# Performance work log

Measured on AMD Instinct MI355X. Metric: run time of the kernel, lower is better.

## Reference

```python
import jax, jax.numpy as jnp
import numpy as np

B, N, H, W, D = 4, 8, 32, 32, 64

def setup_inputs() -> dict:
    key = jax.random.key(0)
    k1, k2, k3, k4 = jax.random.split(key, 4)
    scale = D ** (-0.5)
    q = jax.random.normal(k1, (B, N, H, W, D), dtype=jnp.float32)
    k = jax.random.normal(k2, (B, N, H, W, D), dtype=jnp.float32)
    # learned absolute position embeddings, init N(mean=scale, std=1) per nn.init.normal_(t, scale)
    ph = jax.random.normal(k3, (H, D), dtype=jnp.float32) + scale
    pw = jax.random.normal(k4, (W, D), dtype=jnp.float32) + scale
    return {"q": q, "k": k, "ph": ph, "pw": pw}

def reference(q, k, ph, pw):
    # content-content logits: [b,n,H,W,H,W]
    logits = jnp.einsum('bnhwd,bnpqd->bnhwpq', q, k)
    # absolute positional bias: emb[p,q,d] = ph[p,d] + pw[q,d]
    emb = ph[:, None, :] + pw[None, :, :]            # [H, W, D]
    logits = logits + jnp.einsum('bnxyd,pqd->bnxypq', q, emb)
    return logits
```

## Files before the change

### kernel.cpp

```cpp
#include <hip/hip_runtime.h>


typedef __bf16 bf16x8 __attribute__((ext_vector_type(8)));
typedef __bf16 bf16x4 __attribute__((ext_vector_type(4)));
typedef float  f32x16 __attribute__((ext_vector_type(16)));

#define LDSTRIDE 72

__global__ __launch_bounds__(512)
void abs_pos_emb_gemm(const float* __restrict__ q,
                      const float* __restrict__ k,
                      const float* __restrict__ ph,
                      const float* __restrict__ pw,
                      float* __restrict__ out)
{
    extern __shared__ __bf16 lds[];
    __bf16* As  = lds;
    __bf16* Bs0 = lds + 256 * LDSTRIDE;
    __bf16* Bs1 = lds + 320 * LDSTRIDE;

    const int tid = threadIdx.x;
    const int bid = blockIdx.x;
    const int batch = ((bid & 7) << 2) + (bid >> 6);
    const int j     = (bid >> 3) & 7;
    const int trow  = (j >> 1) << 8;
    const int tcol0 = (j & 1) << 9;

    const float* Qb = q + (size_t)batch * (1024 * 64);
    const float* Kb = k + (size_t)batch * (1024 * 64);
    float* Ob = out + (size_t)batch * (1024u * 1024u);

#pragma unroll
    for (int i = 0; i < 8; ++i) {
        int f   = i * 512 + tid;
        int row = f >> 4;
        int col = (f & 15) << 2;
        float4 v = *reinterpret_cast<const float4*>(
            Qb + (size_t)(trow + row) * 64 + col);
        bf16x4 h;
        h[0] = (__bf16)v.x; h[1] = (__bf16)v.y;
        h[2] = (__bf16)v.z; h[3] = (__bf16)v.w;
        *reinterpret_cast<bf16x4*>(&As[row * LDSTRIDE + col]) = h;
    }

#pragma unroll
    for (int i = 0; i < 2; ++i) {
        int f   = i * 512 + tid;
        int row = f >> 4;
        int col = (f & 15) << 2;
        int grow = tcol0 + row;
        int p  = grow >> 5;
        int qq = grow & 31;
        float4 v  = *reinterpret_cast<const float4*>(Kb + (size_t)grow * 64 + col);
        float4 vp = *reinterpret_cast<const float4*>(ph + p  * 64 + col);
        float4 vw = *reinterpret_cast<const float4*>(pw + qq * 64 + col);
        bf16x4 h;
        h[0] = (__bf16)(v.x + vp.x + vw.x);
        h[1] = (__bf16)(v.y + vp.y + vw.y);
        h[2] = (__bf16)(v.z + vp.z + vw.z);
        h[3] = (__bf16)(v.w + vp.w + vw.w);
        *reinterpret_cast<bf16x4*>(&Bs0[row * LDSTRIDE + col]) = h;
    }

    __syncthreads();

    const int lane = tid & 63;
    const int wid  = tid >> 6;
    const int wrow = (wid >> 1) << 6;
    const int wcl  = (wid & 1)  << 5;
    const int fr   = lane & 31;
    const int fk   = (lane >> 5) << 3;
    const int srow = trow + wrow + ((lane >> 5) << 2);

    const int prow0 = tid >> 4;
    const int prow1 = prow0 + 32;
    const int pcol  = (tid & 15) << 2;

#pragma unroll
    for (int c = 0; c < 8; ++c) {
        const __bf16* B  = (c & 1) ? Bs1 : Bs0;
        __bf16*       Bn = (c & 1) ? Bs0 : Bs1;

        float4 kv0, kv1, vp0, vp1, vw0, vw1;
        if (c < 7) {
            int g0 = tcol0 + (c + 1) * 64 + prow0;
            int g1 = tcol0 + (c + 1) * 64 + prow1;
            kv0 = *reinterpret_cast<const float4*>(Kb + (size_t)g0 * 64 + pcol);
            kv1 = *reinterpret_cast<const float4*>(Kb + (size_t)g1 * 64 + pcol);
            vp0 = *reinterpret_cast<const float4*>(ph + (g0 >> 5) * 64 + pcol);
            vp1 = *reinterpret_cast<const float4*>(ph + (g1 >> 5) * 64 + pcol);
            vw0 = *reinterpret_cast<const float4*>(pw + (g0 & 31) * 64 + pcol);
            vw1 = *reinterpret_cast<const float4*>(pw + (g1 & 31) * 64 + pcol);
        }

        f32x16 acc0 = {};
        f32x16 acc1 = {};
#pragma unroll
        for (int kk = 0; kk < 4; ++kk) {
            const int kb = kk * 16 + fk;
            bf16x8 a0 = *reinterpret_cast<const bf16x8*>(&As[(wrow      + fr) * LDSTRIDE + kb]);
            bf16x8 a1 = *reinterpret_cast<const bf16x8*>(&As[(wrow + 32 + fr) * LDSTRIDE + kb]);
            bf16x8 b0 = *reinterpret_cast<const bf16x8*>(&B [(wcl       + fr) * LDSTRIDE + kb]);
            acc0 = __builtin_amdgcn_mfma_f32_32x32x16_bf16(a0, b0, acc0, 0, 0, 0);
            acc1 = __builtin_amdgcn_mfma_f32_32x32x16_bf16(a1, b0, acc1, 0, 0, 0);
        }

        {
            const int scol = tcol0 + (c << 6) + wcl + fr;
#pragma unroll
            for (int r = 0; r < 16; ++r) {
                int roff = (r & 3) + ((r >> 2) << 3);
                Ob[(size_t)(srow + roff) * 1024 + scol]      = acc0[r];
            }
#pragma unroll
            for (int r = 0; r < 16; ++r) {
                int roff = (r & 3) + ((r >> 2) << 3);
                Ob[(size_t)(srow + 32 + roff) * 1024 + scol] = acc1[r];
            }
        }

        if (c < 7) {
            bf16x4 h0, h1;
            h0[0] = (__bf16)(kv0.x + vp0.x + vw0.x);
            h0[1] = (__bf16)(kv0.y + vp0.y + vw0.y);
            h0[2] = (__bf16)(kv0.z + vp0.z + vw0.z);
            h0[3] = (__bf16)(kv0.w + vp0.w + vw0.w);
            h1[0] = (__bf16)(kv1.x + vp1.x + vw1.x);
            h1[1] = (__bf16)(kv1.y + vp1.y + vw1.y);
            h1[2] = (__bf16)(kv1.z + vp1.z + vw1.z);
            h1[3] = (__bf16)(kv1.w + vp1.w + vw1.w);
            *reinterpret_cast<bf16x4*>(&Bn[prow0 * LDSTRIDE + pcol]) = h0;
            *reinterpret_cast<bf16x4*>(&Bn[prow1 * LDSTRIDE + pcol]) = h1;
            __syncthreads();
        }
    }
}

extern "C" void kernel_launch(void* const* d_in, const int* in_sizes, int n_in,
                              void* d_out, int out_size, void* d_ws, size_t ws_size,
                              hipStream_t stream) {
    const float* q  = (const float*)d_in[0];
    const float* k  = (const float*)d_in[1];
    const float* ph = (const float*)d_in[2];
    const float* pw = (const float*)d_in[3];
    float* out = (float*)d_out;

    size_t lds_bytes = (256u + 128u) * LDSTRIDE * sizeof(__bf16);
    hipLaunchKernelGGL(abs_pos_emb_gemm, dim3(256), dim3(512), lds_bytes, stream,
                       q, k, ph, pw, out);
}
```

Measured before the change: 28.68 us.

## Retile to 128-row by full-width blocks with register-held A fragments

Each block now covers 128 query rows across all 1024 key columns instead of 256 rows by 512 columns. Each wave now holds one 32x32 accumulator rather than two. The A operand fragments are loaded from LDS into registers once, before the column loop, instead of on every chunk. LDS use shrinks, and the barrier is replaced by an explicit lgkmcnt wait plus s_barrier. In exchange, every block must recompute the full K+emb staging for all 1024 columns, which doubles the global K loads per block, and there are fewer MFMAs per barrier.

```diff
diff --git a/kernel.cpp b/kernel.cpp
--- a/kernel.cpp
+++ b/kernel.cpp
@@ -16,22 +16,21 @@
 {
     extern __shared__ __bf16 lds[];
     __bf16* As  = lds;
-    __bf16* Bs0 = lds + 256 * LDSTRIDE;
-    __bf16* Bs1 = lds + 320 * LDSTRIDE;
+    __bf16* Bs0 = lds + 128 * LDSTRIDE;
+    __bf16* Bs1 = lds + 192 * LDSTRIDE;
 
     const int tid = threadIdx.x;
     const int bid = blockIdx.x;
     const int batch = ((bid & 7) << 2) + (bid >> 6);
     const int j     = (bid >> 3) & 7;
-    const int trow  = (j >> 1) << 8;
-    const int tcol0 = (j & 1) << 9;
+    const int trow  = j << 7;
 
     const float* Qb = q + (size_t)batch * (1024 * 64);
     const float* Kb = k + (size_t)batch * (1024 * 64);
     float* Ob = out + (size_t)batch * (1024u * 1024u);
 
 #pragma unroll
-    for (int i = 0; i < 8; ++i) {
+    for (int i = 0; i < 4; ++i) {
         int f   = i * 512 + tid;
         int row = f >> 4;
         int col = (f & 15) << 2;
@@ -48,10 +47,9 @@
         int f   = i * 512 + tid;
         int row = f >> 4;
         int col = (f & 15) << 2;
-        int grow = tcol0 + row;
-        int p  = grow >> 5;
-        int qq = grow & 31;
-        float4 v  = *reinterpret_cast<const float4*>(Kb + (size_t)grow * 64 + col);
+        int p  = row >> 5;
+        int qq = row & 31;
+        float4 v  = *reinterpret_cast<const float4*>(Kb + (size_t)row * 64 + col);
         float4 vp = *reinterpret_cast<const float4*>(ph + p  * 64 + col);
         float4 vw = *reinterpret_cast<const float4*>(pw + qq * 64 + col);
         bf16x4 h;
@@ -66,25 +64,32 @@
 
     const int lane = tid & 63;
     const int wid  = tid >> 6;
-    const int wrow = (wid >> 1) << 6;
+    const int wrow = (wid >> 1) << 5;
     const int wcl  = (wid & 1)  << 5;
     const int fr   = lane & 31;
     const int fk   = (lane >> 5) << 3;
     const int srow = trow + wrow + ((lane >> 5) << 2);
+
+    bf16x8 afrag[4];
+#pragma unroll
+    for (int kk = 0; kk < 4; ++kk) {
+        afrag[kk] = *reinterpret_cast<const bf16x8*>(
+            &As[(wrow + fr) * LDSTRIDE + kk * 16 + fk]);
+    }
 
     const int prow0 = tid >> 4;
     const int prow1 = prow0 + 32;
     const int pcol  = (tid & 15) << 2;
 
 #pragma unroll
-    for (int c = 0; c < 8; ++c) {
+    for (int c = 0; c < 16; ++c) {
         const __bf16* B  = (c & 1) ? Bs1 : Bs0;
         __bf16*       Bn = (c & 1) ? Bs0 : Bs1;
 
         float4 kv0, kv1, vp0, vp1, vw0, vw1;
-        if (c < 7) {
-            int g0 = tcol0 + (c + 1) * 64 + prow0;
-            int g1 = tcol0 + (c + 1) * 64 + prow1;
+        if (c < 15) {
+            int g0 = (c + 1) * 64 + prow0;
+            int g1 = (c + 1) * 64 + prow1;
             kv0 = *reinterpret_cast<const float4*>(Kb + (size_t)g0 * 64 + pcol);
             kv1 = *reinterpret_cast<const float4*>(Kb + (size_t)g1 * 64 + pcol);
             vp0 = *reinterpret_cast<const float4*>(ph + (g0 >> 5) * 64 + pcol);
@@ -93,33 +98,24 @@
             vw1 = *reinterpret_cast<const float4*>(pw + (g1 & 31) * 64 + pcol);
         }
 
-        f32x16 acc0 = {};
-        f32x16 acc1 = {};
+        f32x16 acc = {};
 #pragma unroll
         for (int kk = 0; kk < 4; ++kk) {
-            const int kb = kk * 16 + fk;
-            bf16x8 a0 = *reinterpret_cast<const bf16x8*>(&As[(wrow      + fr) * LDSTRIDE + kb]);
-            bf16x8 a1 = *reinterpret_cast<const bf16x8*>(&As[(wrow + 32 + fr) * LDSTRIDE + kb]);
-            bf16x8 b0 = *reinterpret_cast<const bf16x8*>(&B [(wcl       + fr) * LDSTRIDE + kb]);
-            acc0 = __builtin_amdgcn_mfma_f32_32x32x16_bf16(a0, b0, acc0, 0, 0, 0);
-            acc1 = __builtin_amdgcn_mfma_f32_32x32x16_bf16(a1, b0, acc1, 0, 0, 0);
+            bf16x8 b0 = *reinterpret_cast<const bf16x8*>(
+                &B[(wcl + fr) * LDSTRIDE + kk * 16 + fk]);
+            acc = __builtin_amdgcn_mfma_f32_32x32x16_bf16(afrag[kk], b0, acc, 0, 0, 0);
         }
 
         {
-            const int scol = tcol0 + (c << 6) + wcl + fr;
+            const int scol = (c << 6) + wcl + fr;
 #pragma unroll
             for (int r = 0; r < 16; ++r) {
                 int roff = (r & 3) + ((r >> 2) << 3);
-                Ob[(size_t)(srow + roff) * 1024 + scol]      = acc0[r];
-            }
-#pragma unroll
-            for (int r = 0; r < 16; ++r) {
-                int roff = (r & 3) + ((r >> 2) << 3);
-                Ob[(size_t)(srow + 32 + roff) * 1024 + scol] = acc1[r];
+                Ob[(size_t)(srow + roff) * 1024 + scol] = acc[r];
             }
         }
 
-        if (c < 7) {
+        if (c < 15) {
             bf16x4 h0, h1;
             h0[0] = (__bf16)(kv0.x + vp0.x + vw0.x);
             h0[1] = (__bf16)(kv0.y + vp0.y + vw0.y);
@@ -131,7 +127,8 @@
             h1[3] = (__bf16)(kv1.w + vp1.w + vw1.w);
             *reinterpret_cast<bf16x4*>(&Bn[prow0 * LDSTRIDE + pcol]) = h0;
             *reinterpret_cast<bf16x4*>(&Bn[prow1 * LDSTRIDE + pcol]) = h1;
-            __syncthreads();
+            asm volatile("s_waitcnt lgkmcnt(0)" ::: "memory");
+            __builtin_amdgcn_s_barrier();
         }
     }
 }
@@ -145,7 +142,7 @@
     const float* pw = (const float*)d_in[3];
     float* out = (float*)d_out;
 
-    size_t lds_bytes = (256u + 128u) * LDSTRIDE * sizeof(__bf16);
+    size_t lds_bytes = (128u + 128u) * LDSTRIDE * sizeof(__bf16);
     hipLaunchKernelGGL(abs_pos_emb_gemm, dim3(256), dim3(512), lds_bytes, stream,
                        q, k, ph, pw, out);
 }
```

After: 34.06 us. +18.8%, slower.
